# Performance work log

Measured on AMD Instinct MI355X. Metric: run time of the kernel, lower is better.

Reference implementation:

```python
import jax, jax.numpy as jnp
import numpy as np

B, QL, D = 4, 1024, 1024
H, HD = 16, 64
KVL = 2048


def setup_inputs() -> dict:
    key = jax.random.key(0)
    ks = jax.random.split(key, 6)
    scale = 1.0 / np.sqrt(D)
    return {
        "hidden_states": jax.random.normal(ks[0], (B, QL, D), dtype=jnp.float32),
        "key_states": jax.random.normal(ks[1], (B, H, KVL, HD), dtype=jnp.float32),
        "value_states": jax.random.normal(ks[2], (B, H, KVL, HD), dtype=jnp.float32),
        "attention_mask": jnp.zeros((B, 1, 1, KVL), dtype=jnp.float32),
        "Wq": jax.random.normal(ks[3], (D, D), dtype=jnp.float32) * scale,
        "Wo": jax.random.normal(ks[4], (D, D), dtype=jnp.float32) * scale,
    }


def reference(hidden_states, key_states, value_states, attention_mask, Wq, Wo):
    batch = hidden_states.shape[0]
    # Q projection (T5 Linear has no bias), split heads: [B, H, Q, HD]
    q = jnp.einsum("bqd,de->bqe", hidden_states, Wq)
    q = q.reshape(batch, -1, H, HD).transpose(0, 2, 1, 3)
    # NOTE: T5 attention has NO 1/sqrt(d) scaling
    scores = jnp.einsum("bhqd,bhkd->bhqk", q, key_states) + attention_mask
    attn = jax.nn.softmax(scores.astype(jnp.float32), axis=-1).astype(scores.dtype)
    out = jnp.einsum("bhqk,bhkd->bhqd", attn, value_states)
    out = out.transpose(0, 2, 1, 3).reshape(batch, -1, H * HD)
    return jnp.einsum("bqe,ed->bqd", out, Wo)
```

## Files before the change

### kernel.cpp

```cpp
#include <hip/hip_runtime.h>
#include <hip/hip_bf16.h>
#include <hip/hip_fp16.h>
#include <stdint.h>

typedef _Float16 f16;
typedef _Float16 f16x2 __attribute__((ext_vector_type(2)));
typedef _Float16 f16x4 __attribute__((ext_vector_type(4)));
typedef _Float16 f16x8 __attribute__((ext_vector_type(8)));
typedef float f32x4 __attribute__((ext_vector_type(4)));
typedef float f32x16 __attribute__((ext_vector_type(16)));

#define B_ 4
#define QL_ 1024
#define D_ 1024
#define H_ 16
#define HD_ 64
#define KVL_ 2048
#define L2E 1.44269504088896f

__device__ __forceinline__ void g2lds16(const void* g, void* l) {
    __builtin_amdgcn_global_load_lds(
        (const __attribute__((address_space(1))) uint32_t*)g,
        (__attribute__((address_space(3))) uint32_t*)l,
        16, 0, 0);
}

union U8 { uint32_t u[4]; f16x8 v; };

__device__ __forceinline__ uint32_t pkrtz(float a, float b) {
    auto t = __builtin_amdgcn_cvt_pkrtz(a, b);
    return __builtin_bit_cast(uint32_t, t);
}

__global__ void preprocess(const float* __restrict__ hs, f16* __restrict__ hs_h,
                           const float* __restrict__ K, f16* __restrict__ K_h,
                           const float* __restrict__ Wq, f16* __restrict__ Wq_t,
                           const float* __restrict__ Wo, f16* __restrict__ Wo_t,
                           const float* __restrict__ V, f16* __restrict__ V_t,
                           const float* __restrict__ mask, float* __restrict__ mL) {
    __shared__ float t[64][65];
    int bid = blockIdx.x, tid = threadIdx.x;
    if (bid < 1024) {
        const int n4 = (B_ * QL_ * D_) / 4;
        for (int i = bid * 256 + tid; i < n4; i += 1024 * 256) {
            float4 v = ((const float4*)hs)[i];
            f16x4 o = { (f16)v.x, (f16)v.y, (f16)v.z, (f16)v.w };
            ((f16x4*)hs_h)[i] = o;
        }
    } else if (bid < 3072) {
        int t0 = (bid - 1024) * 256 + tid;
#pragma unroll
        for (int rep = 0; rep < 2; ++rep) {
            int U = t0 + rep * 524288;
            int bh = U >> 14, rem = U & 16383;
            int ch = rem >> 9, r2 = rem & 511;
            int dsl = r2 >> 7, r3 = r2 & 127;
            int kv = r3 >> 1, hi2 = r3 & 1;
            const float* sp = K + (((size_t)bh * KVL_ + ch * 64 + kv) * HD_ + dsl * 16 + hi2 * 8);
            f16x8 o;
#pragma unroll
            for (int j = 0; j < 8; ++j) o[j] = (f16)sp[j];
            *(f16x8*)(K_h + (size_t)U * 8) = o;
        }
    } else if (bid < 3584) {
        int wbid = bid - 3072;
        const float* src = wbid < 256 ? Wq : Wo;
        f16* dst = wbid < 256 ? Wq_t : Wo_t;
        int b2 = wbid & 255;
        int k0 = (b2 >> 4) << 6, n0 = (b2 & 15) << 6;
        int rr = tid >> 4, c4 = (tid & 15) << 2;
#pragma unroll
        for (int i = 0; i < 4; ++i) {
            int r = i * 16 + rr;
            float4 v = *(const float4*)(src + (size_t)(k0 + r) * 1024 + n0 + c4);
            t[r][c4 + 0] = v.x; t[r][c4 + 1] = v.y; t[r][c4 + 2] = v.z; t[r][c4 + 3] = v.w;
        }
        __syncthreads();
#pragma unroll
        for (int i = 0; i < 4; ++i) {
            int n = i * 16 + rr;
            f16x4 o;
#pragma unroll
            for (int j = 0; j < 4; ++j) o[j] = (f16)t[c4 + j][n];
            *(f16x4*)(dst + (size_t)(n0 + n) * 1024 + k0 + c4) = o;
        }
    } else if (bid < 5632) {
        int vb = bid - 3584;
        int bh = vb >> 5, ch = vb & 31;
        int rr = tid >> 4, c4 = (tid & 15) << 2;
#pragma unroll
        for (int i = 0; i < 4; ++i) {
            int r = i * 16 + rr;
            float4 v = *(const float4*)(V + ((size_t)bh * KVL_ + ch * 64 + r) * HD_ + c4);
            t[r][c4 + 0] = v.x; t[r][c4 + 1] = v.y; t[r][c4 + 2] = v.z; t[r][c4 + 3] = v.w;
        }
        __syncthreads();
#pragma unroll
        for (int rep = 0; rep < 2; ++rep) {
            int u = tid + rep * 256;
            int st = u >> 7, d = (u >> 1) & 63, hi2 = u & 1;
            f16x8 o;
#pragma unroll
            for (int j = 0; j < 8; ++j) {
                int kvl = st * 16 + (j & 3) + 8 * (j >> 2) + 4 * hi2;
                o[j] = (f16)t[kvl][d];
            }
            *(f16x8*)(V_t + ((size_t)(bh * 32 + ch) * 512 + u) * 8) = o;
        }
    } else {
        int i = (bid - 5632) * 256 + tid;
        if (i < (B_ * KVL_) / 4) {
            f32x4 v = ((const f32x4*)mask)[i];
            v *= L2E;
            ((f32x4*)mL)[i] = v;
        }
    }
}

template <int EPI>
__global__ __launch_bounds__(512) void gemm_tn(
    const f16* __restrict__ A, const f16* __restrict__ BT, void* __restrict__ Cout,
    int M, int N, int K) {
    __shared__ char Alds[2][16384];
    __shared__ char Blds[2][8192];
    int d0 = blockIdx.x;
    int xcd = d0 & 7, sx = d0 >> 3;
    int bm = xcd * 4 + (sx & 3);
    int bn = sx >> 2;
    int tid = threadIdx.x, w = tid >> 6, l = tid & 63;
    int l15 = l & 15, lg = l >> 4;
    int wm = w >> 1, wn = w & 1;
    f32x4 acc[2][2] = {};

    const char* ag0; const char* ag1; int ao0, ao1;
    {
        int i0 = w, i1 = w + 8;
        int r0 = i0 * 8 + (l >> 3), r1 = i1 * 8 + (l >> 3);
        int c0 = (l & 7) ^ (r0 & 7), c1 = (l & 7) ^ (r1 & 7);
        ag0 = (const char*)A + ((size_t)(bm * 128 + r0) * K + c0 * 8) * 2;
        ag1 = (const char*)A + ((size_t)(bm * 128 + r1) * K + c1 * 8) * 2;
        ao0 = i0 * 1024; ao1 = i1 * 1024;
    }
    int rB = w * 8 + (l >> 3);
    int ccB = (l & 7) ^ (rB & 7);
    const char* bgp = (const char*)BT + ((size_t)(bn * 64 + rB) * K + ccB * 8) * 2;
    int boB = w * 1024;

    int aoff[2][2], boff[2][2];
#pragma unroll
    for (int ks = 0; ks < 2; ++ks)
#pragma unroll
        for (int m = 0; m < 2; ++m) {
            int ra = wm * 32 + m * 16 + l15;
            aoff[ks][m] = ra * 128 + ((ks * 64 + lg * 16) ^ ((ra & 7) << 4));
            int rb = wn * 32 + m * 16 + l15;
            boff[ks][m] = rb * 128 + ((ks * 64 + lg * 16) ^ ((rb & 7) << 4));
        }
    const char* Ab = &Alds[0][0];
    const char* Bb = &Blds[0][0];

#define GSTAGE(buf, soff)                                      \
    {                                                          \
        g2lds16(ag0 + (soff), &Alds[buf][ao0]);                \
        g2lds16(ag1 + (soff), &Alds[buf][ao1]);                \
        g2lds16(bgp + (soff), &Blds[buf][boB]);                \
    }
#define GCOMP(buf)                                                               \
    _Pragma("unroll") for (int ks = 0; ks < 2; ++ks) {                           \
        f16x8 af[2], bf[2];                                                      \
        af[0] = *(const f16x8*)(Ab + (buf) * 16384 + aoff[ks][0]);               \
        af[1] = *(const f16x8*)(Ab + (buf) * 16384 + aoff[ks][1]);               \
        bf[0] = *(const f16x8*)(Bb + (buf) * 8192 + boff[ks][0]);                \
        bf[1] = *(const f16x8*)(Bb + (buf) * 8192 + boff[ks][1]);                \
        _Pragma("unroll") for (int m = 0; m < 2; ++m)                            \
            _Pragma("unroll") for (int n = 0; n < 2; ++n)                        \
                acc[m][n] = __builtin_amdgcn_mfma_f32_16x16x32_f16(af[m], bf[n], acc[m][n], 0, 0, 0); \
    }

    GSTAGE(0, 0);
    asm volatile("s_waitcnt vmcnt(0)" ::: "memory");
    __syncthreads();

    for (int t2 = 0; t2 < 8; ++t2) {
        GSTAGE(1, 128);
        GCOMP(0);
        asm volatile("s_waitcnt vmcnt(0)" ::: "memory");
        __syncthreads();
        if (t2 < 7) GSTAGE(0, 256);
        GCOMP(1);
        asm volatile("s_waitcnt vmcnt(0)" ::: "memory");
        __syncthreads();
        ag0 += 256; ag1 += 256; bgp += 256;
    }

#pragma unroll
    for (int m = 0; m < 2; ++m)
#pragma unroll
        for (int n = 0; n < 2; ++n)
#pragma unroll
            for (int i = 0; i < 4; ++i) {
                int row = bm * 128 + wm * 32 + m * 16 + lg * 4 + i;
                int col = bn * 64 + wn * 32 + n * 16 + l15;
                if (EPI == 0) {
                    float v = acc[m][n][i] * L2E;
                    int b = row >> 10, q = row & 1023, h = col >> 6, d = col & 63;
                    ((f16*)Cout)[(((size_t)b * H_ + h) * QL_ + q) * HD_ + d] = (f16)v;
                } else {
                    ((float*)Cout)[(size_t)row * N + col] = acc[m][n][i];
                }
            }
#undef GSTAGE
#undef GCOMP
}

__global__ __launch_bounds__(512, 4) void attn_fused(
    const f16* __restrict__ qh, const f16* __restrict__ kh, const f16* __restrict__ vt,
    const float* __restrict__ mL, f16* __restrict__ aout) {
    __shared__ char lds_buf[65536];
    __shared__ float frl[8][32];
    __shared__ float fr2[4][2][32];
    __shared__ float2 msx[4][32];

    int tid = threadIdx.x, w = tid >> 6, l = tid & 63;
    int l31 = l & 31, hi = l >> 5;
    int g = w >> 2, wg = w & 3;
    int d0 = blockIdx.x;
    int xcd = d0 & 7, sx = d0 >> 3;
    int bh = xcd * 8 + (sx & 7);
    int qt = sx >> 3;
    int b = bh >> 4, h = bh & 15;

    const char* lbase = lds_buf + g * 32768 + l31 * 32 + hi * 16;

    f16x8 Qf[4];
    {
        const f16* qp = qh + ((size_t)bh * QL_ + qt * 128 + wg * 32 + l31) * HD_ + hi * 8;
#pragma unroll
        for (int ds_ = 0; ds_ < 4; ++ds_) Qf[ds_] = *(const f16x8*)(qp + ds_ * 16);
    }

    int i0 = wg * 2;
    const char* kgp0 = (const char*)kh + (((size_t)(bh * 32 + g * 16) * 512) + i0 * 64 + l) * 16;
    const char* kgp1 = kgp0 + 1024;
    const char* vgp0 = (const char*)vt + (((size_t)(bh * 32 + g * 16) * 512) + i0 * 64 + l) * 16;
    const char* vgp1 = vgp0 + 1024;
    char* kl0 = lds_buf + g * 32768 + i0 * 1024;
    char* kl1 = kl0 + 1024;
    char* vl0 = lds_buf + g * 32768 + 16384 + i0 * 1024;
    char* vl1 = vl0 + 1024;

#define PREF(buf, soff)                                  \
    {                                                    \
        g2lds16(kgp0 + (soff), kl0 + (buf) * 8192);      \
        g2lds16(kgp1 + (soff), kl1 + (buf) * 8192);      \
        g2lds16(vgp0 + (soff), vl0 + (buf) * 8192);      \
        g2lds16(vgp1 + (soff), vl1 + (buf) * 8192);      \
    }

    float mrun = -1e30f, ssum = 0.f;
    f32x16 acc[2] = {};
    const float* mp = mL + b * KVL_ + g * 1024;
    const f16x2 one2 = { (f16)1.0f, (f16)1.0f };

#define BODY(buf, mo)                                                                     \
    _Pragma("unroll") for (int kb = 0; kb < 2; ++kb) {                                    \
        f32x16 St;                                                                        \
        _Pragma("unroll") for (int g4 = 0; g4 < 4; ++g4) {                                \
            f32x4 mv = *(const f32x4*)(mp + (mo) + kb * 32 + g4 * 8 + hi * 4);            \
            St[g4 * 4 + 0] = mv[0]; St[g4 * 4 + 1] = mv[1];                               \
            St[g4 * 4 + 2] = mv[2]; St[g4 * 4 + 3] = mv[3];                               \
        }                                                                                 \
        __builtin_amdgcn_s_setprio(1);                                                    \
        _Pragma("unroll") for (int ds_ = 0; ds_ < 4; ++ds_) {                             \
            f16x8 kf = *(const f16x8*)(lbase + (buf) * 8192 + ds_ * 2048 + kb * 1024);    \
            St = __builtin_amdgcn_mfma_f32_32x32x16_f16(kf, Qf[ds_], St, 0, 0, 0);        \
        }                                                                                 \
        __builtin_amdgcn_s_setprio(0);                                                    \
        float a0 = fmaxf(fmaxf(St[0], St[1]), St[2]);                                     \
        float a1 = fmaxf(fmaxf(St[3], St[4]), St[5]);                                     \
        float a2 = fmaxf(fmaxf(St[6], St[7]), St[8]);                                     \
        float a3 = fmaxf(fmaxf(St[9], St[10]), St[11]);                                   \
        float a4 = fmaxf(fmaxf(St[12], St[13]), St[14]);                                  \
        float pm = fmaxf(fmaxf(fmaxf(a0, a1), St[15]), fmaxf(fmaxf(a2, a3), a4));         \
        pm = fmaxf(pm, __shfl_xor(pm, 32));                                               \
        if (__any(pm > mrun + 12.f)) {                                                    \
            float mn = fmaxf(mrun, pm);                                                   \
            float fac = exp2f(mrun - mn);                                                 \
            mrun = mn; ssum *= fac;                                                       \
            frl[w][l31] = fac;                                                            \
            asm volatile("s_waitcnt lgkmcnt(0)" ::: "memory");                            \
            _Pragma("unroll") for (int g4 = 0; g4 < 4; ++g4) {                            \
                f32x4 fv = *(const f32x4*)&frl[w][g4 * 8 + hi * 4];                       \
                _Pragma("unroll") for (int c = 0; c < 2; ++c)                             \
                    _Pragma("unroll") for (int j = 0; j < 4; ++j)                         \
                        acc[c][g4 * 4 + j] *= fv[j];                                      \
            }                                                                             \
        }                                                                                 \
        uint32_t pk[8];                                                                   \
        _Pragma("unroll") for (int i = 0; i < 8; ++i) {                                   \
            float p0 = exp2f(St[2 * i] - mrun);                                           \
            float p1 = exp2f(St[2 * i + 1] - mrun);                                       \
            uint32_t u = pkrtz(p0, p1);                                                   \
            pk[i] = u;                                                                    \
            ssum = __builtin_amdgcn_fdot2(__builtin_bit_cast(f16x2, u), one2, ssum, false); \
        }                                                                                 \
        __builtin_amdgcn_s_setprio(1);                                                    \
        _Pragma("unroll") for (int sti = 0; sti < 2; ++sti) {                             \
            U8 pa;                                                                        \
            pa.u[0] = pk[sti * 4 + 0]; pa.u[1] = pk[sti * 4 + 1];                         \
            pa.u[2] = pk[sti * 4 + 2]; pa.u[3] = pk[sti * 4 + 3];                         \
            const int st_ = kb * 2 + sti;                                                 \
            _Pragma("unroll") for (int c = 0; c < 2; ++c) {                               \
                U8 vb;                                                                    \
                vb.v = *(const f16x8*)(lbase + 16384 + (buf) * 8192 + st_ * 2048 + c * 1024); \
                acc[c] = __builtin_amdgcn_mfma_f32_32x32x16_f16(pa.v, vb.v, acc[c], 0, 0, 0); \
            }                                                                             \
        }                                                                                 \
        __builtin_amdgcn_s_setprio(0);                                                    \
    }

    PREF(0, 0);
    asm volatile("s_waitcnt vmcnt(0)" ::: "memory");
    __syncthreads();

    for (int it = 0; it < 8; ++it) {
        PREF(1, 8192);
        BODY(0, 0);
        asm volatile("s_waitcnt vmcnt(0)" ::: "memory");
        __syncthreads();
        if (it < 7) PREF(0, 16384);
        BODY(1, 64);
        asm volatile("s_waitcnt vmcnt(0)" ::: "memory");
        __syncthreads();
        kgp0 += 16384; kgp1 += 16384; vgp0 += 16384; vgp1 += 16384;
        mp += 128;
    }

    ssum += __shfl_xor(ssum, 32);
    char* exch = lds_buf;
    if (g == 1) {
        int base = (wg * 64 + l) * 128;
#pragma unroll
        for (int i = 0; i < 8; ++i) {
            int c = i >> 2, j0 = (i & 3) * 4;
            f32x4 vv = { acc[c][j0], acc[c][j0 + 1], acc[c][j0 + 2], acc[c][j0 + 3] };
            *(f32x4*)(exch + base + ((i * 16) ^ ((l & 7) << 4))) = vv;
        }
        if (hi == 0) msx[wg][l31] = make_float2(mrun, ssum);
    }
    __syncthreads();
    if (g == 0) {
        float2 mb = msx[wg][l31];
        float m = fmaxf(mrun, mb.x);
        float fA = exp2f(mrun - m), fB = exp2f(mb.x - m);
        float s = ssum * fA + mb.y * fB;
        float rinv = 1.0f / s;
        if (hi == 0) { fr2[wg][0][l31] = fA * rinv; fr2[wg][1][l31] = fB * rinv; }
        asm volatile("s_waitcnt lgkmcnt(0)" ::: "memory");
        int base = (wg * 64 + l) * 128;
#pragma unroll
        for (int c = 0; c < 2; ++c)
#pragma unroll
            for (int g4 = 0; g4 < 4; ++g4) {
                f32x4 gAv = *(const f32x4*)&fr2[wg][0][g4 * 8 + hi * 4];
                f32x4 gBv = *(const f32x4*)&fr2[wg][1][g4 * 8 + hi * 4];
                int i = c * 4 + g4;
                f32x4 pv = *(const f32x4*)(exch + base + ((i * 16) ^ ((l & 7) << 4)));
#pragma unroll
                for (int j = 0; j < 4; ++j) {
                    float o = acc[c][g4 * 4 + j] * gAv[j] + pv[j] * gBv[j];
                    int q = qt * 128 + wg * 32 + g4 * 8 + hi * 4 + j;
                    int dd = c * 32 + l31;
                    aout[((size_t)b * QL_ + q) * D_ + h * HD_ + dd] = (f16)o;
                }
            }
    }
#undef PREF
#undef BODY
}

extern "C" void kernel_launch(void* const* d_in, const int* in_sizes, int n_in,
                              void* d_out, int out_size, void* d_ws, size_t ws_size,
                              hipStream_t stream) {
    const float* hs = (const float*)d_in[0];
    const float* K  = (const float*)d_in[1];
    const float* V  = (const float*)d_in[2];
    const float* mask = (const float*)d_in[3];
    const float* Wq = (const float*)d_in[4];
    const float* Wo = (const float*)d_in[5];
    float* out = (float*)d_out;
    char* ws = (char*)d_ws;

    f16* hs_h = (f16*)(ws + 0);
    f16* Wq_t = (f16*)(ws + 8388608);
    f16* Wo_t = (f16*)(ws + 10485760);
    f16* K_h  = (f16*)(ws + 12582912);
    f16* V_t  = (f16*)(ws + 29360128);
    f16* q_h  = (f16*)(ws + 46137344);
    f16* a_o  = (f16*)(ws + 54525952);
    float* mL = (float*)(ws + 62914560);

    preprocess<<<5640, 256, 0, stream>>>(hs, hs_h, K, K_h, Wq, Wq_t, Wo, Wo_t,
                                         V, V_t, mask, mL);
    gemm_tn<0><<<512, 512, 0, stream>>>(hs_h, Wq_t, (void*)q_h, 4096, 1024, 1024);
    attn_fused<<<512, 512, 0, stream>>>(q_h, K_h, V_t, mL, a_o);
    gemm_tn<1><<<512, 512, 0, stream>>>(a_o, Wo_t, (void*)out, 4096, 1024, 1024);
}
```

Measured before the change: 117.4 us.

## Stage mask in LDS and issue both QK^T MFMA groups before softmax

The attention mask row is copied into LDS once per block, using the asynchronous global-to-LDS load, instead of being read from global memory inside every inner iteration. Each 64-key chunk now issues all eight QK^T MFMAs for both 32-key halves before either softmax/PV step runs, which lets matrix work overlap the exp and max code. The cross-half shuffle for the row max is moved inside the rare rescale branch. This adds 8 KB of LDS per block, which may reduce occupancy, and holds two score accumulators live at once, which raises register pressure.

```diff
diff --git a/kernel.cpp b/kernel.cpp
--- a/kernel.cpp
+++ b/kernel.cpp
@@ -217,6 +217,7 @@
     const f16* __restrict__ qh, const f16* __restrict__ kh, const f16* __restrict__ vt,
     const float* __restrict__ mL, f16* __restrict__ aout) {
     __shared__ char lds_buf[65536];
+    __shared__ float msk[2][1024];
     __shared__ float frl[8][32];
     __shared__ float fr2[4][2][32];
     __shared__ float2 msx[4][32];
@@ -231,6 +232,7 @@
     int b = bh >> 4, h = bh & 15;
 
     const char* lbase = lds_buf + g * 32768 + l31 * 32 + hi * 16;
+    const char* mlb = (const char*)&msk[g][0] + hi * 16;
 
     f16x8 Qf[4];
     {
@@ -259,31 +261,18 @@
 
     float mrun = -1e30f, ssum = 0.f;
     f32x16 acc[2] = {};
-    const float* mp = mL + b * KVL_ + g * 1024;
     const f16x2 one2 = { (f16)1.0f, (f16)1.0f };
 
-#define BODY(buf, mo)                                                                     \
-    _Pragma("unroll") for (int kb = 0; kb < 2; ++kb) {                                    \
-        f32x16 St;                                                                        \
-        _Pragma("unroll") for (int g4 = 0; g4 < 4; ++g4) {                                \
-            f32x4 mv = *(const f32x4*)(mp + (mo) + kb * 32 + g4 * 8 + hi * 4);            \
-            St[g4 * 4 + 0] = mv[0]; St[g4 * 4 + 1] = mv[1];                               \
-            St[g4 * 4 + 2] = mv[2]; St[g4 * 4 + 3] = mv[3];                               \
-        }                                                                                 \
-        __builtin_amdgcn_s_setprio(1);                                                    \
-        _Pragma("unroll") for (int ds_ = 0; ds_ < 4; ++ds_) {                             \
-            f16x8 kf = *(const f16x8*)(lbase + (buf) * 8192 + ds_ * 2048 + kb * 1024);    \
-            St = __builtin_amdgcn_mfma_f32_32x32x16_f16(kf, Qf[ds_], St, 0, 0, 0);        \
-        }                                                                                 \
-        __builtin_amdgcn_s_setprio(0);                                                    \
+#define SMPV(St, buf, stbase)                                                             \
+    {                                                                                     \
         float a0 = fmaxf(fmaxf(St[0], St[1]), St[2]);                                     \
         float a1 = fmaxf(fmaxf(St[3], St[4]), St[5]);                                     \
         float a2 = fmaxf(fmaxf(St[6], St[7]), St[8]);                                     \
         float a3 = fmaxf(fmaxf(St[9], St[10]), St[11]);                                   \
         float a4 = fmaxf(fmaxf(St[12], St[13]), St[14]);                                  \
-        float pm = fmaxf(fmaxf(fmaxf(a0, a1), St[15]), fmaxf(fmaxf(a2, a3), a4));         \
-        pm = fmaxf(pm, __shfl_xor(pm, 32));                                               \
-        if (__any(pm > mrun + 12.f)) {                                                    \
+        float lmax = fmaxf(fmaxf(fmaxf(a0, a1), St[15]), fmaxf(a2, fmaxf(a3, a4)));       \
+        if (__any(lmax > mrun + 12.f)) {                                                  \
+            float pm = fmaxf(lmax, __shfl_xor(lmax, 32));                                 \
             float mn = fmaxf(mrun, pm);                                                   \
             float fac = exp2f(mrun - mn);                                                 \
             mrun = mn; ssum *= fac;                                                       \
@@ -309,7 +298,7 @@
             U8 pa;                                                                        \
             pa.u[0] = pk[sti * 4 + 0]; pa.u[1] = pk[sti * 4 + 1];                         \
             pa.u[2] = pk[sti * 4 + 2]; pa.u[3] = pk[sti * 4 + 3];                         \
-            const int st_ = kb * 2 + sti;                                                 \
+            const int st_ = (stbase) + sti;                                               \
             _Pragma("unroll") for (int c = 0; c < 2; ++c) {                               \
                 U8 vb;                                                                    \
                 vb.v = *(const f16x8*)(lbase + 16384 + (buf) * 8192 + st_ * 2048 + c * 1024); \
@@ -319,21 +308,47 @@
         __builtin_amdgcn_s_setprio(0);                                                    \
     }
 
+#define CHUNK(buf, mo)                                                                    \
+    {                                                                                     \
+        f32x16 St0, St1;                                                                  \
+        _Pragma("unroll") for (int g4 = 0; g4 < 4; ++g4) {                                \
+            f32x4 m0 = *(const f32x4*)(mlb + (mo) + g4 * 32);                             \
+            f32x4 m1 = *(const f32x4*)(mlb + (mo) + 128 + g4 * 32);                       \
+            St0[g4 * 4 + 0] = m0[0]; St0[g4 * 4 + 1] = m0[1];                             \
+            St0[g4 * 4 + 2] = m0[2]; St0[g4 * 4 + 3] = m0[3];                             \
+            St1[g4 * 4 + 0] = m1[0]; St1[g4 * 4 + 1] = m1[1];                             \
+            St1[g4 * 4 + 2] = m1[2]; St1[g4 * 4 + 3] = m1[3];                             \
+        }                                                                                 \
+        __builtin_amdgcn_s_setprio(1);                                                    \
+        _Pragma("unroll") for (int ds_ = 0; ds_ < 4; ++ds_) {                             \
+            f16x8 kf = *(const f16x8*)(lbase + (buf) * 8192 + ds_ * 2048);                \
+            St0 = __builtin_amdgcn_mfma_f32_32x32x16_f16(kf, Qf[ds_], St0, 0, 0, 0);      \
+        }                                                                                 \
+        _Pragma("unroll") for (int ds_ = 0; ds_ < 4; ++ds_) {                             \
+            f16x8 kf = *(const f16x8*)(lbase + (buf) * 8192 + ds_ * 2048 + 1024);         \
+            St1 = __builtin_amdgcn_mfma_f32_32x32x16_f16(kf, Qf[ds_], St1, 0, 0, 0);      \
+        }                                                                                 \
+        __builtin_amdgcn_s_setprio(0);                                                    \
+        SMPV(St0, buf, 0);                                                                \
+        SMPV(St1, buf, 2);                                                                \
+    }
+
+    g2lds16((const char*)(mL + b * KVL_ + g * 1024 + wg * 256), (char*)&msk[g][wg * 256]);
     PREF(0, 0);
     asm volatile("s_waitcnt vmcnt(0)" ::: "memory");
     __syncthreads();
 
     for (int it = 0; it < 8; ++it) {
         PREF(1, 8192);
-        BODY(0, 0);
+        CHUNK(0, 0);
         asm volatile("s_waitcnt vmcnt(0)" ::: "memory");
         __syncthreads();
         if (it < 7) PREF(0, 16384);
-        BODY(1, 64);
+        CHUNK(1, 256);
         asm volatile("s_waitcnt vmcnt(0)" ::: "memory");
         __syncthreads();
         kgp0 += 16384; kgp1 += 16384; vgp0 += 16384; vgp1 += 16384;
-        mp += 128;
+        mlb += 512;
     }
 
     ssum += __shfl_xor(ssum, 32);
@@ -376,7 +391,8 @@
             }
     }
 #undef PREF
-#undef BODY
+#undef SMPV
+#undef CHUNK
 }
 
 extern "C" void kernel_launch(void* const* d_in, const int* in_sizes, int n_in,
```

New measurement: 117.2 us. About the same (-0.2%).
